# Optimization experiments

Hardware: AMD Instinct MI355X
Metric: run time of the kernel (lower is better)

## Reference

```python
import jax, jax.numpy as jnp
import numpy as np

B, S, HID = 1, 2048, 2048
H = 16
DN, DR, DV = 128, 64, 128          # qk_nope_head_dim, qk_rope_head_dim, v_head_dim
DQ = DN + DR                        # q_head_dim = 192
QLR, KVLR = 1536, 512               # q_lora_rank, kv_lora_rank
MAXP = 32 * 1024
SCALE = DQ ** -0.5
EPS = 1e-6


def rmsnorm(x, w):
    return x * jax.lax.rsqrt(jnp.mean(x * x, axis=-1, keepdims=True) + EPS) * w


def rotate_half(x):
    h = x.shape[-1] // 2
    return jnp.concatenate((-x[..., h:], x[..., :h]), axis=-1)


def interleave_to_half(x):
    # torch: view(b,h,s,d//2,2).transpose(4,3).reshape(b,h,s,d)
    b, h, s, d = x.shape
    return x.reshape(b, h, s, d // 2, 2).transpose(0, 1, 2, 4, 3).reshape(b, h, s, d)


def setup_inputs() -> dict:
    key = jax.random.key(0)
    ks = jax.random.split(key, 8)
    def w(k, shape):
        fan_in = shape[-1]
        return jax.random.normal(k, shape, jnp.float32) * (fan_in ** -0.5)
    inp = {
        "hidden_states": jax.random.normal(ks[0], (B, S, HID), jnp.float32),
        "q_a_w": w(ks[1], (QLR, HID)),
        "q_a_ln": jnp.ones((QLR,), jnp.float32),
        "q_b_w": w(ks[2], (H * DQ, QLR)),
        "kv_a_w": w(ks[3], (KVLR + DR, HID)),
        "kv_a_ln": jnp.ones((KVLR,), jnp.float32),
        "kv_b_w": w(ks[4], (H * (DN + DV), KVLR)),
        "o_w": w(ks[5], (HID, H * DV)),
    }
    # rotary tables, seq_len = 32k
    inv_freq = 1.0 / (10000.0 ** (np.arange(0, DR, 2, dtype=np.float32) / DR))
    t = np.arange(MAXP, dtype=np.float32)
    freqs = np.outer(t, inv_freq)
    emb = np.concatenate((freqs, freqs), axis=-1)
    inp["cos"] = jnp.asarray(np.cos(emb), jnp.float32)
    inp["sin"] = jnp.asarray(np.sin(emb), jnp.float32)
    # bool mask, True = masked (causal)
    inp["attention_mask"] = jnp.triu(jnp.ones((S, S), bool), 1)[None, None]
    inp["position_ids"] = jnp.arange(S, dtype=jnp.int64 if jax.config.jax_enable_x64 else jnp.int32)[None].repeat(B, 0)
    return inp


def reference(hidden_states, q_a_w, q_a_ln, q_b_w, kv_a_w, kv_a_ln, kv_b_w, o_w,
              cos, sin, attention_mask, position_ids):
    b, s, _ = hidden_states.shape
    # low-rank Q: q_b(LN(q_a(x)))
    q = rmsnorm(hidden_states @ q_a_w.T, q_a_ln) @ q_b_w.T         # [b,s,H*DQ]
    q = q.reshape(b, s, H, DQ).transpose(0, 2, 1, 3)               # [b,H,s,DQ]
    q_nope, q_pe = q[..., :DN], q[..., DN:]
    # compressed KV + decoupled rope key
    ckv = hidden_states @ kv_a_w.T                                  # [b,s,KVLR+DR]
    compressed_kv, k_pe = ckv[..., :KVLR], ckv[..., KVLR:]
    k_pe = k_pe.reshape(b, s, 1, DR).transpose(0, 2, 1, 3)          # [b,1,s,DR]
    kv = rmsnorm(compressed_kv, kv_a_ln) @ kv_b_w.T                 # [b,s,H*(DN+DV)]
    kv = kv.reshape(b, s, H, DN + DV).transpose(0, 2, 1, 3)         # [b,H,s,DN+DV]
    k_nope, value_states = kv[..., :DN], kv[..., DN:]
    # rotary with interleaved->half reorder on the rope slice only
    cos_p = cos[position_ids][:, None]                              # [b,1,s,DR]
    sin_p = sin[position_ids][:, None]
    q_pe = interleave_to_half(q_pe)
    k_pe = interleave_to_half(k_pe)
    q_pe = q_pe * cos_p + rotate_half(q_pe) * sin_p
    k_pe = k_pe * cos_p + rotate_half(k_pe) * sin_p
    query_states = jnp.concatenate((q_nope, q_pe), axis=-1)         # [b,H,s,DQ]
    key_states = jnp.concatenate(
        (k_nope, jnp.broadcast_to(k_pe, (b, H, s, DR))), axis=-1)   # [b,H,s,DQ]
    # manual attention
    scores = jnp.einsum("bhqd,bhkd->bhqk", query_states, key_states) * SCALE
    scores = jnp.where(attention_mask, jnp.float32(-10000.0), scores)
    attn = jax.nn.softmax(scores.astype(jnp.float32), axis=-1).astype(query_states.dtype)
    attn_out = jnp.einsum("bhqk,bhkd->bhqd", attn, value_states)    # [b,H,s,DV]
    attn_out = attn_out.transpose(0, 2, 1, 3).reshape(b, s, H * DV)
    return attn_out @ o_w.T                                         # [b,s,HID]
```

## Files before the change

### kernel.cpp

```cpp
#include <hip/hip_runtime.h>
#include <stdint.h>

typedef unsigned short u16;
typedef __attribute__((ext_vector_type(8))) short short8;
typedef __attribute__((ext_vector_type(4))) float f32x4;
typedef __attribute__((ext_vector_type(4))) unsigned short ushort4_t;
typedef __attribute__((ext_vector_type(4))) float float4_t;

#define DEV_INLINE __device__ __forceinline__

DEV_INLINE u16 f2bf(float f) {
    union { float f; unsigned u; } x; x.f = f;
    unsigned u = x.u;
    unsigned r = (u + 0x7FFFu + ((u >> 16) & 1u)) >> 16;
    return (u16)r;
}

DEV_INLINE float bf2f(u16 b) {
    union { unsigned u; float f; } x; x.u = ((unsigned)b) << 16;
    return x.f;
}

DEV_INLINE float fexp2(float x) {
    float r;
    asm("v_exp_f32 %0, %1" : "=v"(r) : "v"(x));
    return r;
}

DEV_INLINE unsigned cvtpk_bf16(float lo, float hi) {
    unsigned r;
    asm("v_cvt_pk_bf16_f32 %0, %1, %2" : "=v"(r) : "v"(lo), "v"(hi));
    return r;
}

template <int CTRL>
DEV_INLINE float dppmaxf(float x) {
    union { float f; int i; } u; u.f = x;
    int y = __builtin_amdgcn_update_dpp(u.i, u.i, CTRL, 0xf, 0xf, true);
    union { int i; float f; } v; v.i = y;
    return fmaxf(x, v.f);
}

DEV_INLINE float dpp_xor1(float x) {
    union { float f; int i; } u; u.f = x;
    int y = __builtin_amdgcn_update_dpp(u.i, u.i, 0xB1, 0xf, 0xf, true);
    union { int i; float f; } v; v.i = y;
    return v.f;
}

DEV_INLINE float rmax16(float x) {
    x = dppmaxf<0xB1>(x);
    x = dppmaxf<0x4E>(x);
    x = dppmaxf<0x141>(x);
    x = dppmaxf<0x140>(x);
    return x;
}

__global__ void conv_all(const float* __restrict__ s0, u16* __restrict__ d0, long e0,
                         const float* __restrict__ s1, u16* __restrict__ d1, long e1,
                         const float* __restrict__ s2, u16* __restrict__ d2, long e2,
                         const float* __restrict__ s3, u16* __restrict__ d3, long e3,
                         const float* __restrict__ s4, u16* __restrict__ d4, long e4,
                         const float* __restrict__ s5, u16* __restrict__ d5, long e5,
                         int rows_valid, int cols4) {
    long i = (long)blockIdx.x * 256 + threadIdx.x;
    if (i >= e5) return;
    if (i >= e4) {
        long j = i - e4;
        long row = j / cols4;
        ushort4_t o; o.x = 0; o.y = 0; o.z = 0; o.w = 0;
        if (row < rows_valid) {
            float4_t v = ((const float4_t*)s5)[j];
            o.x = f2bf(v.x); o.y = f2bf(v.y); o.z = f2bf(v.z); o.w = f2bf(v.w);
        }
        ((ushort4_t*)d5)[j] = o;
        return;
    }
    const float* s; u16* d; long base;
    if      (i < e0) { s = s0; d = d0; base = 0; }
    else if (i < e1) { s = s1; d = d1; base = e0; }
    else if (i < e2) { s = s2; d = d2; base = e1; }
    else if (i < e3) { s = s3; d = d3; base = e2; }
    else             { s = s4; d = d4; base = e3; }
    long j = i - base;
    float4_t v = ((const float4_t*)s)[j];
    ushort4_t o;
    o.x = f2bf(v.x); o.y = f2bf(v.y); o.z = f2bf(v.z); o.w = f2bf(v.w);
    ((ushort4_t*)d)[j] = o;
}

#define BK 32

DEV_INLINE void gload16(const u16* g, u16* l) {
    __builtin_amdgcn_global_load_lds((const __attribute__((address_space(1))) unsigned int*)g,
                                     (__attribute__((address_space(3))) unsigned int*)l,
                                     16, 0, 0);
}

template <typename OT>
__global__ __launch_bounds__(256) void gemm64_db(const u16* __restrict__ A, const u16* __restrict__ B,
                                                 OT* __restrict__ C, int M, int N, int K) {
    __shared__ u16 As[2][64 * BK];
    __shared__ u16 Bs[2][128 * BK];
    const int tid = threadIdx.x;
    const int wid = tid >> 6, lane = tid & 63;
    const int lm = lane & 15, lk = lane >> 4;
    const long bm = (long)blockIdx.y * 64, bn = (long)blockIdx.x * 128;

    f32x4 acc[4][2] = {};

    const int rowS = lane >> 2;
    const int colS = ((lane & 3) ^ ((lane >> 3) & 3)) * 8;
    const int cs = (lm >> 1) & 3;
    const u16* Ag = A + (bm + wid * 16 + rowS) * (long)K + colS;
    const u16* Bg = B + (bn + wid * 32 + rowS) * (long)K + colS;
    const int aoff = wid * 16 * BK;
    const int boff = wid * 32 * BK;

    gload16(Ag, &As[0][aoff]);
    gload16(Bg, &Bs[0][boff]);
    gload16(Bg + 16 * (long)K, &Bs[0][boff + 16 * BK]);
    __syncthreads();

    int cur = 0;
    for (int k0 = 0; k0 < K; k0 += BK) {
        if (k0 + BK < K) {
            gload16(Ag + k0 + BK, &As[cur ^ 1][aoff]);
            gload16(Bg + k0 + BK, &Bs[cur ^ 1][boff]);
            gload16(Bg + 16 * (long)K + k0 + BK, &Bs[cur ^ 1][boff + 16 * BK]);
        }
        short8 af[4], bfr[2];
#pragma unroll
        for (int m = 0; m < 4; ++m)
            af[m] = *(const short8*)&As[cur][(m * 16 + lm) * BK + (lk ^ cs) * 8];
#pragma unroll
        for (int n = 0; n < 2; ++n)
            bfr[n] = *(const short8*)&Bs[cur][(wid * 32 + n * 16 + lm) * BK + (lk ^ cs) * 8];
#pragma unroll
        for (int m = 0; m < 4; ++m)
#pragma unroll
            for (int n = 0; n < 2; ++n)
                acc[m][n] = __builtin_amdgcn_mfma_f32_16x16x32_bf16(af[m], bfr[n], acc[m][n], 0, 0, 0);
        __syncthreads();
        cur ^= 1;
    }

#pragma unroll
    for (int m = 0; m < 4; ++m)
#pragma unroll
        for (int n = 0; n < 2; ++n)
#pragma unroll
            for (int r = 0; r < 4; ++r) {
                long idx = (bm + m * 16 + lk * 4 + r) * (long)N + bn + wid * 32 + n * 16 + lm;
                if constexpr (sizeof(OT) == 4) C[idx] = acc[m][n][r];
                else                           C[idx] = f2bf(acc[m][n][r]);
            }
}

__global__ __launch_bounds__(256) void gemm_qkv(const u16* __restrict__ qnA, const u16* __restrict__ qbB,
                                                const u16* __restrict__ kvnA, const u16* __restrict__ kvbB,
                                                u16* __restrict__ Qb, u16* __restrict__ Kb, u16* __restrict__ Vt,
                                                const int* __restrict__ pos,
                                                const float* __restrict__ cosT, const float* __restrict__ sinT) {
    __shared__ u16 SMEM[12288];
    u16* As = SMEM;
    u16* Bs = SMEM + 4096;
    const int tid = threadIdx.x;
    const int wid = tid >> 6, lane = tid & 63;
    const int lm = lane & 15, lk = lane >> 4;

    const bool isq = blockIdx.x < 768;
    const int gx = isq ? blockIdx.x : blockIdx.x - 768;
    const int nb = isq ? 24 : 32;
    const int K  = isq ? 1536 : 512;
    const u16* A = isq ? qnA : kvnA;
    const u16* B = isq ? qbB : kvbB;
    const long bn = (long)(gx % nb) * 128;
    const long bm = (long)(gx / nb) * 64;

    f32x4 acc[4][2] = {};

    const int rowS = lane >> 2;
    const int colS = ((lane & 3) ^ ((lane >> 3) & 3)) * 8;
    const int cs = (lm >> 1) & 3;
    const u16* Ag = A + (bm + wid * 16 + rowS) * (long)K + colS;
    const u16* Bg = B + (bn + wid * 32 + rowS) * (long)K + colS;
    const int aoff = wid * 16 * BK;
    const int boff = wid * 32 * BK;

    gload16(Ag, &As[aoff]);
    gload16(Bg, &Bs[boff]);
    gload16(Bg + 16 * (long)K, &Bs[boff + 16 * BK]);
    __syncthreads();

    int cur = 0;
    for (int k0 = 0; k0 < K; k0 += BK) {
        if (k0 + BK < K) {
            gload16(Ag + k0 + BK, &As[(cur ^ 1) * 2048 + aoff]);
            gload16(Bg + k0 + BK, &Bs[(cur ^ 1) * 4096 + boff]);
            gload16(Bg + 16 * (long)K + k0 + BK, &Bs[(cur ^ 1) * 4096 + boff + 16 * BK]);
        }
        short8 af[4], bfr[2];
#pragma unroll
        for (int m = 0; m < 4; ++m)
            af[m] = *(const short8*)&As[cur * 2048 + (m * 16 + lm) * BK + (lk ^ cs) * 8];
#pragma unroll
        for (int n = 0; n < 2; ++n)
            bfr[n] = *(const short8*)&Bs[cur * 4096 + (wid * 32 + n * 16 + lm) * BK + (lk ^ cs) * 8];
#pragma unroll
        for (int m = 0; m < 4; ++m)
#pragma unroll
            for (int n = 0; n < 2; ++n)
                acc[m][n] = __builtin_amdgcn_mfma_f32_16x16x32_bf16(af[m], bfr[n], acc[m][n], 0, 0, 0);
        __syncthreads();
        cur ^= 1;
    }

    if (isq) {
#pragma unroll
        for (int n = 0; n < 2; ++n) {
            const int c = (int)bn + wid * 32 + n * 16 + lm;
            const int h = c / 192;
            const int d = c - h * 192;
            const bool pe = (d >= 128);
            const int t = (d - 128) >> 1;
#pragma unroll
            for (int m = 0; m < 4; ++m)
#pragma unroll
                for (int r = 0; r < 4; ++r) {
                    const long row = bm + m * 16 + lk * 4 + r;
                    float own = acc[m][n][r];
                    float par = dpp_xor1(own);
                    float val = own;
                    if (pe) {
                        long p = pos[row];
                        float cc = cosT[p * 64 + t];
                        float ss = sinT[p * 64 + t];
                        val = (d & 1) ? own * cc + par * ss : own * cc - par * ss;
                    }
                    Qb[((long)h * 2048 + row) * 192 + d] = f2bf(val);
                }
        }
    } else {
        const int hh = (gx & 31) >> 1;
        const bool isV = (gx & 1) != 0;
        if (!isV) {
#pragma unroll
            for (int m = 0; m < 4; ++m)
#pragma unroll
                for (int n = 0; n < 2; ++n)
#pragma unroll
                    for (int r = 0; r < 4; ++r)
                        Kb[((long)hh * 2048 + bm + m * 16 + lk * 4 + r) * 192 + wid * 32 + n * 16 + lm]
                            = f2bf(acc[m][n][r]);
        } else {
            __syncthreads();
            u16* Ls = SMEM;
#pragma unroll
            for (int n = 0; n < 2; ++n) {
                int d = wid * 32 + n * 16 + lm;
                int swz = ((d >> 3) & 7) << 3;
#pragma unroll
                for (int m = 0; m < 4; ++m)
#pragma unroll
                    for (int r = 0; r < 4; ++r) {
                        int row = m * 16 + lk * 4 + r;
                        Ls[d * 72 + (row ^ swz)] = f2bf(acc[m][n][r]);
                    }
            }
            __syncthreads();
#pragma unroll
            for (int i = 0; i < 8; ++i) {
                int u = i * 256 + tid;
                int d = u >> 4, s4 = (u & 15) * 4;
                int swz = ((d >> 3) & 7) << 3;
                ushort4_t v;
                v.x = Ls[d * 72 + ((s4 + 0) ^ swz)]; v.y = Ls[d * 72 + ((s4 + 1) ^ swz)];
                v.z = Ls[d * 72 + ((s4 + 2) ^ swz)]; v.w = Ls[d * 72 + ((s4 + 3) ^ swz)];
                *(ushort4_t*)(Vt + ((long)hh * 128 + d) * 2048 + bm + s4) = v;
            }
        }
    }
}

__global__ __launch_bounds__(256) void norm_rope(const float* __restrict__ qkva,
                                                 const float* __restrict__ q_ln,
                                                 const float* __restrict__ kv_ln,
                                                 u16* __restrict__ qn, u16* __restrict__ kvn,
                                                 const int* __restrict__ pos,
                                                 const float* __restrict__ cosT,
                                                 const float* __restrict__ sinT,
                                                 u16* __restrict__ Kb) {
    const int b = blockIdx.x, tid = threadIdx.x;
    if (b < 4096) {
        const bool isq = b < 2048;
        const int row = isq ? b : b - 2048;
        const int ncols = isq ? 1536 : 512;
        const float* x = qkva + (long)row * 2176 + (isq ? 0 : 1536);
        const float* w = isq ? q_ln : kv_ln;
        u16* out = isq ? (qn + (long)row * 1536) : (kvn + (long)row * 512);
        float ss = 0.f;
        for (int c = tid; c < ncols; c += 256) { float v = x[c]; ss = fmaf(v, v, ss); }
#pragma unroll
        for (int off = 32; off > 0; off >>= 1) ss += __shfl_down(ss, off);
        __shared__ float part[4];
        if ((tid & 63) == 0) part[tid >> 6] = ss;
        __syncthreads();
        float tot = part[0] + part[1] + part[2] + part[3];
        float rs = rsqrtf(tot / (float)ncols + 1e-6f);
        for (int c = tid; c < ncols; c += 256) out[c] = f2bf(x[c] * rs * w[c]);
    } else {
        int idx = (b - 4096) * 256 + tid;
        int s = idx >> 5, j = idx & 31;
        long p = pos[s];
        const float* row = qkva + (long)s * 2176 + 2048;
        float x0 = row[2 * j], x1 = row[2 * j + 1];
        float c0 = cosT[p * 64 + j], s0 = sinT[p * 64 + j];
        u16 o0 = f2bf(x0 * c0 - x1 * s0);
        u16 o1 = f2bf(x1 * c0 + x0 * s0);
#pragma unroll
        for (int h = 0; h < 16; ++h) {
            u16* kr = Kb + ((long)h * 2048 + s) * 192 + 128;
            kr[2 * j] = o0; kr[2 * j + 1] = o1;
        }
    }
}

__global__ __launch_bounds__(512) void attn_fwd(const u16* __restrict__ Qb, const u16* __restrict__ Kb,
                                                const u16* __restrict__ Vt, u16* __restrict__ Ao) {
    __shared__ __align__(16) char smem[92672];

    const int b = blockIdx.x;
    const int h = (b & 7) * 2 + ((b >> 3) & 1);
    const int pi = b >> 4;
    const int tid = threadIdx.x;
    const int wid = tid >> 6, lane = tid & 63;
    const int lm = lane & 15, lk = lane >> 4;
    const int s = wid >> 2, wp = wid & 3;
    const int t256 = tid & 255;

    u16* Ks0 = (u16*)smem + s * 12288;
    u16* Vs0 = (u16*)(smem + 49152) + s * 8192;
    u16* PsW = (u16*)(smem + 81920) + wid * 640;
    float* ML = (float*)(smem + 92160);
    float* Ob = (float*)smem;

    const u16* Kh = Kb + (long)h * 2048 * 192;
    const u16* Vh = Vt + (long)h * 128 * 2048;

    short8 bones = {};
    if (lm == 0) {
#pragma unroll
        for (int j = 0; j < 8; ++j) bones[j] = (short)0x3F80;
    }
    const float C2 = 0.104117548f;

    for (int half = 0; half < 2; ++half) {
        const int qi = half ? (31 - pi) : pi;
        const int q0 = qi * 64;
        const int nt = 2 * qi + 2;
        const int niter = qi + 1;

        short8 qf[6];
        const u16* qbase = Qb + ((long)h * 2048 + q0 + wp * 16 + lm) * 192;
#pragma unroll
        for (int kf = 0; kf < 6; ++kf) qf[kf] = *(const short8*)(qbase + kf * 32 + lk * 8);

        f32x4 o[8] = {};
        f32x4 o9 = {};
        float mrow[4] = {-1e30f, -1e30f, -1e30f, -1e30f};

        short8 kreg[3], vreg[2];
        {
            const long k0 = s * 32;
#pragma unroll
            for (int i = 0; i < 3; ++i) {
                int idx = i * 256 + t256; int r = idx / 24, c = (idx % 24) * 8;
                kreg[i] = *(const short8*)(Kh + (k0 + r) * 192 + c);
            }
#pragma unroll
            for (int i = 0; i < 2; ++i) {
                int idx = i * 256 + t256; int dv = idx >> 2, kvb = idx & 3;
                vreg[i] = *(const short8*)(Vh + (long)dv * 2048 + k0 + kvb * 8);
            }
#pragma unroll
            for (int i = 0; i < 3; ++i) {
                int idx = i * 256 + t256; int r = idx / 24, c8 = idx % 24;
                *(short8*)&Ks0[r * 192 + ((c8 ^ (r & 7)) << 3)] = kreg[i];
            }
#pragma unroll
            for (int i = 0; i < 2; ++i) {
                int idx = i * 256 + t256; int dv = idx >> 2, kvb = idx & 3;
                *(short8*)&Vs0[kvb * 1024 + ((dv * 8) ^ (kvb * 16))] = vreg[i];
            }
        }
        __syncthreads();

        int cur = 0;
        for (int it = 0; it < niter; ++it) {
            const int ts = 2 * it + s;
            const int k0 = ts * 32;
            const bool more = (it + 1 < niter);

            if (more) {
                const long k0n = (long)(ts + 2) * 32;
#pragma unroll
                for (int i = 0; i < 3; ++i) {
                    int idx = i * 256 + t256; int r = idx / 24, c = (idx % 24) * 8;
                    kreg[i] = *(const short8*)(Kh + (k0n + r) * 192 + c);
                }
#pragma unroll
                for (int i = 0; i < 2; ++i) {
                    int idx = i * 256 + t256; int dv = idx >> 2, kvb = idx & 3;
                    vreg[i] = *(const short8*)(Vh + (long)dv * 2048 + k0n + kvb * 8);
                }
            }

            const u16* KsC = Ks0 + cur * 6144;
            const u16* VsC = Vs0 + cur * 4096;

            f32x4 sfr[2] = {};
#pragma unroll
            for (int n = 0; n < 2; ++n)
#pragma unroll
                for (int kf = 0; kf < 6; ++kf) {
                    short8 kb = *(const short8*)&KsC[(n * 16 + lm) * 192 + (((kf * 4 + lk) ^ (lm & 7)) << 3)];
                    sfr[n] = __builtin_amdgcn_mfma_f32_16x16x32_bf16(qf[kf], kb, sfr[n], 0, 0, 0);
                }

            float sv[2][4];
            const bool bt = (ts >= nt - 2);
#pragma unroll
            for (int n = 0; n < 2; ++n)
#pragma unroll
                for (int r = 0; r < 4; ++r) {
                    float val = sfr[n][r] * C2;
                    if (bt && (k0 + n * 16 + lm > q0 + wp * 16 + lk * 4 + r)) val = -1e30f;
                    sv[n][r] = val;
                }

            float pmax[4];
#pragma unroll
            for (int r = 0; r < 4; ++r)
                pmax[r] = rmax16(fmaxf(sv[0][r], sv[1][r]));
            bool need = (pmax[0] > mrow[0] + 8.f) || (pmax[1] > mrow[1] + 8.f) ||
                        (pmax[2] > mrow[2] + 8.f) || (pmax[3] > mrow[3] + 8.f);
            if (__any(need)) {
#pragma unroll
                for (int r = 0; r < 4; ++r) {
                    float mnew = fmaxf(mrow[r], pmax[r]);
                    float alpha = fexp2(mrow[r] - mnew);
                    mrow[r] = mnew;
#pragma unroll
                    for (int d = 0; d < 8; ++d) o[d][r] *= alpha;
                    o9[r] *= alpha;
                }
            }
#pragma unroll
            for (int n = 0; n < 2; ++n) {
                float p0 = fexp2(sv[n][0] - mrow[0]);
                float p1 = fexp2(sv[n][1] - mrow[1]);
                float p2 = fexp2(sv[n][2] - mrow[2]);
                float p3 = fexp2(sv[n][3] - mrow[3]);
                unsigned pk01 = cvtpk_bf16(p0, p1);
                unsigned pk23 = cvtpk_bf16(p2, p3);
                int rb = (lk * 4) * 40 + n * 16 + lm;
                PsW[rb]       = (u16)pk01;
                PsW[rb + 40]  = (u16)(pk01 >> 16);
                PsW[rb + 80]  = (u16)pk23;
                PsW[rb + 120] = (u16)(pk23 >> 16);
            }

            short8 pf = *(const short8*)&PsW[lm * 40 + lk * 8];
#pragma unroll
            for (int d = 0; d < 8; ++d) {
                short8 vf = *(const short8*)&VsC[lk * 1024 + (((d * 16 + lm) * 8) ^ (lk * 16))];
                o[d] = __builtin_amdgcn_mfma_f32_16x16x32_bf16(pf, vf, o[d], 0, 0, 0);
            }
            o9 = __builtin_amdgcn_mfma_f32_16x16x32_bf16(pf, bones, o9, 0, 0, 0);

            if (more) {
                u16* KsN = Ks0 + (cur ^ 1) * 6144;
                u16* VsN = Vs0 + (cur ^ 1) * 4096;
#pragma unroll
                for (int i = 0; i < 3; ++i) {
                    int idx = i * 256 + t256; int r = idx / 24, c8 = idx % 24;
                    *(short8*)&KsN[r * 192 + ((c8 ^ (r & 7)) << 3)] = kreg[i];
                }
#pragma unroll
                for (int i = 0; i < 2; ++i) {
                    int idx = i * 256 + t256; int dv = idx >> 2, kvb = idx & 3;
                    *(short8*)&VsN[kvb * 1024 + ((dv * 8) ^ (kvb * 16))] = vreg[i];
                }
            }
            __syncthreads();
            cur ^= 1;
        }

        if (s == 1) {
#pragma unroll
            for (int d = 0; d < 8; ++d)
#pragma unroll
                for (int r = 0; r < 4; ++r)
                    Ob[(wp * 16 + lk * 4 + r) * 128 + d * 16 + lm] = o[d][r];
            if (lm == 0) {
#pragma unroll
                for (int r = 0; r < 4; ++r) {
                    int row = wp * 16 + lk * 4 + r;
                    ML[row * 2 + 0] = mrow[r];
                    ML[row * 2 + 1] = o9[r];
                }
            }
        }
        __syncthreads();
        if (s == 0) {
            float e0[4], e1[4], invl[4];
#pragma unroll
            for (int r = 0; r < 4; ++r) {
                int row = wp * 16 + lk * 4 + r;
                float m1 = ML[row * 2 + 0];
                float l1 = ML[row * 2 + 1];
                float l0 = __shfl(o9[r], lane & 48);
                float M = fmaxf(mrow[r], m1);
                e0[r] = fexp2(mrow[r] - M);
                e1[r] = fexp2(m1 - M);
                invl[r] = 1.f / (l0 * e0[r] + l1 * e1[r]);
            }
#pragma unroll
            for (int d = 0; d < 8; ++d)
#pragma unroll
                for (int r = 0; r < 4; ++r) {
                    int row = wp * 16 + lk * 4 + r;
                    float val = (o[d][r] * e0[r] +
                                 Ob[row * 128 + d * 16 + lm] * e1[r]) * invl[r];
                    Ao[((long)q0 + row) * 2048 + h * 128 + d * 16 + lm] = f2bf(val);
                }
        }
        __syncthreads();
    }
}

extern "C" void kernel_launch(void* const* d_in, const int* in_sizes, int n_in,
                              void* d_out, int out_size, void* d_ws, size_t ws_size,
                              hipStream_t stream) {
    (void)in_sizes; (void)n_in; (void)out_size; (void)ws_size;
    const float* hidden  = (const float*)d_in[0];
    const float* q_a_w   = (const float*)d_in[1];
    const float* q_a_ln  = (const float*)d_in[2];
    const float* q_b_w   = (const float*)d_in[3];
    const float* kv_a_w  = (const float*)d_in[4];
    const float* kv_a_ln = (const float*)d_in[5];
    const float* kv_b_w  = (const float*)d_in[6];
    const float* o_w     = (const float*)d_in[7];
    const float* cosT    = (const float*)d_in[8];
    const float* sinT    = (const float*)d_in[9];
    const int*   pos     = (const int*)d_in[11];

    char* ws = (char*)d_ws;
    u16* o_w_bf   = (u16*)(ws + 0);
    u16* qb_w_bf  = (u16*)(ws + 8388608);
    u16* kvb_w_bf = (u16*)(ws + 17825792);
    u16* qn_bf    = (u16*)(ws + 22020096);
    u16* kvn_bf   = (u16*)(ws + 28311552);
    u16* Qb       = (u16*)(ws + 30408704);
    u16* Kb       = (u16*)(ws + 42991616);
    u16* Vt       = (u16*)(ws + 55574528);
    u16* aout_bf  = (u16*)(ws + 63963136);
    u16*   hid_bf    = (u16*)(ws + 72351744);
    u16*   qkva_w_bf = (u16*)(ws + 80740352);
    float* qkva_f    = (float*)(ws + 89653248);

    conv_all<<<19200, 256, 0, stream>>>(
        hidden, hid_bf,                 1048576L,
        q_a_w,  qkva_w_bf,              1835008L,
        q_b_w,  qb_w_bf,                3014656L,
        kv_b_w, kvb_w_bf,               3538944L,
        o_w,    o_w_bf,                 4587520L,
        kv_a_w, qkva_w_bf + 1536L*2048, 4915200L,
        576, 512);

    gemm64_db<float><<<dim3(17, 32), 256, 0, stream>>>(hid_bf, qkva_w_bf, qkva_f, 2048, 2176, 2048);

    norm_rope<<<4352, 256, 0, stream>>>(qkva_f, q_a_ln, kv_a_ln, qn_bf, kvn_bf, pos, cosT, sinT, Kb);

    gemm_qkv<<<1792, 256, 0, stream>>>(qn_bf, qb_w_bf, kvn_bf, kvb_w_bf, Qb, Kb, Vt, pos, cosT, sinT);

    attn_fwd<<<256, 512, 0, stream>>>(Qb, Kb, Vt, aout_bf);

    gemm64_db<float><<<dim3(16, 32), 256, 0, stream>>>(aout_bf, o_w_bf, (float*)d_out, 2048, 2048, 2048);
}
```

Before: 223.2 us.

## Fuse fp32-to-bf16 conversion into GEMM tile loads, drop standalone convert kernel

Removes the separate conversion kernel that turned the inputs and all weights into bf16 copies. Each GEMM now loads fp32 operands straight from global memory into registers, converts them with packed bf16 instructions, and writes them to LDS after the MFMA step, keeping the double-buffer overlap. This saves one launch and a full extra read/write pass over roughly 20M elements. In exchange, each GEMM tile reads twice the bytes per operand and weight tiles are reloaded and reconverted by every block row, and the async global-to-LDS loads become register-staged loads.

```diff
diff --git a/kernel.cpp b/kernel.cpp
--- a/kernel.cpp
+++ b/kernel.cpp
@@ -6,6 +6,7 @@
 typedef __attribute__((ext_vector_type(4))) float f32x4;
 typedef __attribute__((ext_vector_type(4))) unsigned short ushort4_t;
 typedef __attribute__((ext_vector_type(4))) float float4_t;
+typedef __attribute__((ext_vector_type(4))) unsigned uint4_t;
 
 #define DEV_INLINE __device__ __forceinline__
 
@@ -16,11 +17,6 @@
     return (u16)r;
 }
 
-DEV_INLINE float bf2f(u16 b) {
-    union { unsigned u; float f; } x; x.u = ((unsigned)b) << 16;
-    return x.f;
-}
-
 DEV_INLINE float fexp2(float x) {
     float r;
     asm("v_exp_f32 %0, %1" : "=v"(r) : "v"(x));
@@ -31,6 +27,15 @@
     unsigned r;
     asm("v_cvt_pk_bf16_f32 %0, %1, %2" : "=v"(r) : "v"(lo), "v"(hi));
     return r;
+}
+
+DEV_INLINE void cvt_store8(u16* dst, float4_t lo, float4_t hi) {
+    uint4_t w;
+    w.x = cvtpk_bf16(lo.x, lo.y);
+    w.y = cvtpk_bf16(lo.z, lo.w);
+    w.z = cvtpk_bf16(hi.x, hi.y);
+    w.w = cvtpk_bf16(hi.z, hi.w);
+    *(uint4_t*)dst = w;
 }
 
 template <int CTRL>
@@ -56,39 +61,6 @@
     return x;
 }
 
-__global__ void conv_all(const float* __restrict__ s0, u16* __restrict__ d0, long e0,
-                         const float* __restrict__ s1, u16* __restrict__ d1, long e1,
-                         const float* __restrict__ s2, u16* __restrict__ d2, long e2,
-                         const float* __restrict__ s3, u16* __restrict__ d3, long e3,
-                         const float* __restrict__ s4, u16* __restrict__ d4, long e4,
-                         const float* __restrict__ s5, u16* __restrict__ d5, long e5,
-                         int rows_valid, int cols4) {
-    long i = (long)blockIdx.x * 256 + threadIdx.x;
-    if (i >= e5) return;
-    if (i >= e4) {
-        long j = i - e4;
-        long row = j / cols4;
-        ushort4_t o; o.x = 0; o.y = 0; o.z = 0; o.w = 0;
-        if (row < rows_valid) {
-            float4_t v = ((const float4_t*)s5)[j];
-            o.x = f2bf(v.x); o.y = f2bf(v.y); o.z = f2bf(v.z); o.w = f2bf(v.w);
-        }
-        ((ushort4_t*)d5)[j] = o;
-        return;
-    }
-    const float* s; u16* d; long base;
-    if      (i < e0) { s = s0; d = d0; base = 0; }
-    else if (i < e1) { s = s1; d = d1; base = e0; }
-    else if (i < e2) { s = s2; d = d2; base = e1; }
-    else if (i < e3) { s = s3; d = d3; base = e2; }
-    else             { s = s4; d = d4; base = e3; }
-    long j = i - base;
-    float4_t v = ((const float4_t*)s)[j];
-    ushort4_t o;
-    o.x = f2bf(v.x); o.y = f2bf(v.y); o.z = f2bf(v.z); o.w = f2bf(v.w);
-    ((ushort4_t*)d)[j] = o;
-}
-
 #define BK 32
 
 DEV_INLINE void gload16(const u16* g, u16* l) {
@@ -97,37 +69,125 @@
                                      16, 0, 0);
 }
 
-template <typename OT>
-__global__ __launch_bounds__(256) void gemm64_db(const u16* __restrict__ A, const u16* __restrict__ B,
-                                                 OT* __restrict__ C, int M, int N, int K) {
+__global__ __launch_bounds__(256) void gemm_down(const float* __restrict__ hid,
+                                                 const float* __restrict__ qaw,
+                                                 const float* __restrict__ kvaw,
+                                                 float* __restrict__ C) {
     __shared__ u16 As[2][64 * BK];
     __shared__ u16 Bs[2][128 * BK];
     const int tid = threadIdx.x;
     const int wid = tid >> 6, lane = tid & 63;
     const int lm = lane & 15, lk = lane >> 4;
     const long bm = (long)blockIdx.y * 64, bn = (long)blockIdx.x * 128;
+    const int K = 2048;
 
     f32x4 acc[4][2] = {};
-
+    const int rowS = lane >> 2;
+    const int colS = ((lane & 3) ^ ((lane >> 3) & 3)) * 8;
+    const int cs = (lm >> 1) & 3;
+
+    const float* Ag = hid + (bm + wid * 16 + rowS) * (long)K + colS;
+    const long r0 = bn + wid * 32 + rowS;
+    const long r1 = r0 + 16;
+    const float* Bg0 = (r0 < 1536) ? qaw + r0 * 2048 + colS
+                      : ((r0 - 1536) < 576 ? kvaw + (r0 - 1536) * 2048 + colS : nullptr);
+    const float* Bg1 = (r1 < 1536) ? qaw + r1 * 2048 + colS
+                      : ((r1 - 1536) < 576 ? kvaw + (r1 - 1536) * 2048 + colS : nullptr);
+    const int aoff = wid * 16 * BK + lane * 8;
+    const int boff0 = wid * 32 * BK + lane * 8;
+    const int boff1 = boff0 + 16 * BK;
+
+    const float4_t zf = {0.f, 0.f, 0.f, 0.f};
+    float4_t a0, a1, b00, b01, b10, b11;
+
+#define LOADT(k0)                                                                                  \
+    a0 = *(const float4_t*)(Ag + (k0));                                                            \
+    a1 = *(const float4_t*)(Ag + (k0) + 4);                                                        \
+    if (Bg0) { b00 = *(const float4_t*)(Bg0 + (k0)); b01 = *(const float4_t*)(Bg0 + (k0) + 4); }   \
+    else     { b00 = zf; b01 = zf; }                                                               \
+    if (Bg1) { b10 = *(const float4_t*)(Bg1 + (k0)); b11 = *(const float4_t*)(Bg1 + (k0) + 4); }   \
+    else     { b10 = zf; b11 = zf; }
+
+    LOADT(0);
+    cvt_store8(&As[0][aoff], a0, a1);
+    cvt_store8(&Bs[0][boff0], b00, b01);
+    cvt_store8(&Bs[0][boff1], b10, b11);
+    __syncthreads();
+
+    int cur = 0;
+    for (int k0 = 0; k0 < K; k0 += BK) {
+        const bool more = (k0 + BK < K);
+        if (more) { LOADT(k0 + BK); }
+        short8 af[4], bfr[2];
+#pragma unroll
+        for (int m = 0; m < 4; ++m)
+            af[m] = *(const short8*)&As[cur][(m * 16 + lm) * BK + (lk ^ cs) * 8];
+#pragma unroll
+        for (int n = 0; n < 2; ++n)
+            bfr[n] = *(const short8*)&Bs[cur][(wid * 32 + n * 16 + lm) * BK + (lk ^ cs) * 8];
+#pragma unroll
+        for (int m = 0; m < 4; ++m)
+#pragma unroll
+            for (int n = 0; n < 2; ++n)
+                acc[m][n] = __builtin_amdgcn_mfma_f32_16x16x32_bf16(af[m], bfr[n], acc[m][n], 0, 0, 0);
+        if (more) {
+            cvt_store8(&As[cur ^ 1][aoff], a0, a1);
+            cvt_store8(&Bs[cur ^ 1][boff0], b00, b01);
+            cvt_store8(&Bs[cur ^ 1][boff1], b10, b11);
+        }
+        __syncthreads();
+        cur ^= 1;
+    }
+#undef LOADT
+
+#pragma unroll
+    for (int m = 0; m < 4; ++m)
+#pragma unroll
+        for (int n = 0; n < 2; ++n)
+#pragma unroll
+            for (int r = 0; r < 4; ++r)
+                C[(bm + m * 16 + lk * 4 + r) * 2176L + bn + wid * 32 + n * 16 + lm] = acc[m][n][r];
+}
+
+__global__ __launch_bounds__(256) void gemm_o(const u16* __restrict__ A, const float* __restrict__ B,
+                                              float* __restrict__ C, int M, int N, int K) {
+    __shared__ u16 As[2][64 * BK];
+    __shared__ u16 Bs[2][128 * BK];
+    const int tid = threadIdx.x;
+    const int wid = tid >> 6, lane = tid & 63;
+    const int lm = lane & 15, lk = lane >> 4;
+    const long bm = (long)blockIdx.y * 64, bn = (long)blockIdx.x * 128;
+
+    f32x4 acc[4][2] = {};
     const int rowS = lane >> 2;
     const int colS = ((lane & 3) ^ ((lane >> 3) & 3)) * 8;
     const int cs = (lm >> 1) & 3;
     const u16* Ag = A + (bm + wid * 16 + rowS) * (long)K + colS;
-    const u16* Bg = B + (bn + wid * 32 + rowS) * (long)K + colS;
+    const float* Bg0 = B + (bn + wid * 32 + rowS) * (long)K + colS;
+    const float* Bg1 = Bg0 + 16 * (long)K;
     const int aoff = wid * 16 * BK;
-    const int boff = wid * 32 * BK;
+    const int boff0 = wid * 32 * BK + lane * 8;
+    const int boff1 = boff0 + 16 * BK;
+
+    float4_t b00, b01, b10, b11;
+#define LOADB(k0)                                        \
+    b00 = *(const float4_t*)(Bg0 + (k0));                \
+    b01 = *(const float4_t*)(Bg0 + (k0) + 4);            \
+    b10 = *(const float4_t*)(Bg1 + (k0));                \
+    b11 = *(const float4_t*)(Bg1 + (k0) + 4);
 
     gload16(Ag, &As[0][aoff]);
-    gload16(Bg, &Bs[0][boff]);
-    gload16(Bg + 16 * (long)K, &Bs[0][boff + 16 * BK]);
+    LOADB(0);
+    cvt_store8(&Bs[0][boff0], b00, b01);
+    cvt_store8(&Bs[0][boff1], b10, b11);
     __syncthreads();
 
     int cur = 0;
     for (int k0 = 0; k0 < K; k0 += BK) {
-        if (k0 + BK < K) {
+        const bool more = (k0 + BK < K);
+        if (more) {
             gload16(Ag + k0 + BK, &As[cur ^ 1][aoff]);
-            gload16(Bg + k0 + BK, &Bs[cur ^ 1][boff]);
-            gload16(Bg + 16 * (long)K + k0 + BK, &Bs[cur ^ 1][boff + 16 * BK]);
+            LOADB(k0 + BK);
         }
         short8 af[4], bfr[2];
 #pragma unroll
@@ -141,24 +201,26 @@
 #pragma unroll
             for (int n = 0; n < 2; ++n)
                 acc[m][n] = __builtin_amdgcn_mfma_f32_16x16x32_bf16(af[m], bfr[n], acc[m][n], 0, 0, 0);
+        if (more) {
+            cvt_store8(&Bs[cur ^ 1][boff0], b00, b01);
+            cvt_store8(&Bs[cur ^ 1][boff1], b10, b11);
+        }
         __syncthreads();
         cur ^= 1;
     }
+#undef LOADB
 
 #pragma unroll
     for (int m = 0; m < 4; ++m)
 #pragma unroll
         for (int n = 0; n < 2; ++n)
 #pragma unroll
-            for (int r = 0; r < 4; ++r) {
-                long idx = (bm + m * 16 + lk * 4 + r) * (long)N + bn + wid * 32 + n * 16 + lm;
-                if constexpr (sizeof(OT) == 4) C[idx] = acc[m][n][r];
-                else                           C[idx] = f2bf(acc[m][n][r]);
-            }
-}
-
-__global__ __launch_bounds__(256) void gemm_qkv(const u16* __restrict__ qnA, const u16* __restrict__ qbB,
-                                                const u16* __restrict__ kvnA, const u16* __restrict__ kvbB,
+            for (int r = 0; r < 4; ++r)
+                C[(bm + m * 16 + lk * 4 + r) * (long)N + bn + wid * 32 + n * 16 + lm] = acc[m][n][r];
+}
+
+__global__ __launch_bounds__(256) void gemm_qkv(const u16* __restrict__ qnA, const float* __restrict__ qbw,
+                                                const u16* __restrict__ kvnA, const float* __restrict__ kvbw,
                                                 u16* __restrict__ Qb, u16* __restrict__ Kb, u16* __restrict__ Vt,
                                                 const int* __restrict__ pos,
                                                 const float* __restrict__ cosT, const float* __restrict__ sinT) {
@@ -174,7 +236,7 @@
     const int nb = isq ? 24 : 32;
     const int K  = isq ? 1536 : 512;
     const u16* A = isq ? qnA : kvnA;
-    const u16* B = isq ? qbB : kvbB;
+    const float* Bf = isq ? qbw : kvbw;
     const long bn = (long)(gx % nb) * 128;
     const long bm = (long)(gx / nb) * 64;
 
@@ -184,21 +246,31 @@
     const int colS = ((lane & 3) ^ ((lane >> 3) & 3)) * 8;
     const int cs = (lm >> 1) & 3;
     const u16* Ag = A + (bm + wid * 16 + rowS) * (long)K + colS;
-    const u16* Bg = B + (bn + wid * 32 + rowS) * (long)K + colS;
+    const float* Bg0 = Bf + (bn + wid * 32 + rowS) * (long)K + colS;
+    const float* Bg1 = Bg0 + 16 * (long)K;
     const int aoff = wid * 16 * BK;
-    const int boff = wid * 32 * BK;
+    const int boff0 = wid * 32 * BK + lane * 8;
+    const int boff1 = boff0 + 16 * BK;
+
+    float4_t b00, b01, b10, b11;
+#define LOADB(k0)                                        \
+    b00 = *(const float4_t*)(Bg0 + (k0));                \
+    b01 = *(const float4_t*)(Bg0 + (k0) + 4);            \
+    b10 = *(const float4_t*)(Bg1 + (k0));                \
+    b11 = *(const float4_t*)(Bg1 + (k0) + 4);
 
     gload16(Ag, &As[aoff]);
-    gload16(Bg, &Bs[boff]);
-    gload16(Bg + 16 * (long)K, &Bs[boff + 16 * BK]);
+    LOADB(0);
+    cvt_store8(&Bs[boff0], b00, b01);
+    cvt_store8(&Bs[boff1], b10, b11);
     __syncthreads();
 
     int cur = 0;
     for (int k0 = 0; k0 < K; k0 += BK) {
-        if (k0 + BK < K) {
+        const bool more = (k0 + BK < K);
+        if (more) {
             gload16(Ag + k0 + BK, &As[(cur ^ 1) * 2048 + aoff]);
-            gload16(Bg + k0 + BK, &Bs[(cur ^ 1) * 4096 + boff]);
-            gload16(Bg + 16 * (long)K + k0 + BK, &Bs[(cur ^ 1) * 4096 + boff + 16 * BK]);
+            LOADB(k0 + BK);
         }
         short8 af[4], bfr[2];
 #pragma unroll
@@ -212,9 +284,14 @@
 #pragma unroll
             for (int n = 0; n < 2; ++n)
                 acc[m][n] = __builtin_amdgcn_mfma_f32_16x16x32_bf16(af[m], bfr[n], acc[m][n], 0, 0, 0);
+        if (more) {
+            cvt_store8(&Bs[(cur ^ 1) * 4096 + boff0], b00, b01);
+            cvt_store8(&Bs[(cur ^ 1) * 4096 + boff1], b10, b11);
+        }
         __syncthreads();
         cur ^= 1;
     }
+#undef LOADB
 
     if (isq) {
 #pragma unroll
@@ -557,35 +634,21 @@
     const int*   pos     = (const int*)d_in[11];
 
     char* ws = (char*)d_ws;
-    u16* o_w_bf   = (u16*)(ws + 0);
-    u16* qb_w_bf  = (u16*)(ws + 8388608);
-    u16* kvb_w_bf = (u16*)(ws + 17825792);
-    u16* qn_bf    = (u16*)(ws + 22020096);
-    u16* kvn_bf   = (u16*)(ws + 28311552);
-    u16* Qb       = (u16*)(ws + 30408704);
-    u16* Kb       = (u16*)(ws + 42991616);
-    u16* Vt       = (u16*)(ws + 55574528);
-    u16* aout_bf  = (u16*)(ws + 63963136);
-    u16*   hid_bf    = (u16*)(ws + 72351744);
-    u16*   qkva_w_bf = (u16*)(ws + 80740352);
-    float* qkva_f    = (float*)(ws + 89653248);
-
-    conv_all<<<19200, 256, 0, stream>>>(
-        hidden, hid_bf,                 1048576L,
-        q_a_w,  qkva_w_bf,              1835008L,
-        q_b_w,  qb_w_bf,                3014656L,
-        kv_b_w, kvb_w_bf,               3538944L,
-        o_w,    o_w_bf,                 4587520L,
-        kv_a_w, qkva_w_bf + 1536L*2048, 4915200L,
-        576, 512);
-
-    gemm64_db<float><<<dim3(17, 32), 256, 0, stream>>>(hid_bf, qkva_w_bf, qkva_f, 2048, 2176, 2048);
+    u16*   qn_bf  = (u16*)(ws + 0);
+    u16*   kvn_bf = (u16*)(ws + 6291456);
+    u16*   Qb     = (u16*)(ws + 8388608);
+    u16*   Kb     = (u16*)(ws + 20971520);
+    u16*   Vt     = (u16*)(ws + 33554432);
+    u16*   aout_bf= (u16*)(ws + 41943040);
+    float* qkva_f = (float*)(ws + 50331648);
+
+    gemm_down<<<dim3(17, 32), 256, 0, stream>>>(hidden, q_a_w, kv_a_w, qkva_f);
 
     norm_rope<<<4352, 256, 0, stream>>>(qkva_f, q_a_ln, kv_a_ln, qn_bf, kvn_bf, pos, cosT, sinT, Kb);
 
-    gemm_qkv<<<1792, 256, 0, stream>>>(qn_bf, qb_w_bf, kvn_bf, kvb_w_bf, Qb, Kb, Vt, pos, cosT, sinT);
+    gemm_qkv<<<1792, 256, 0, stream>>>(qn_bf, q_b_w, kvn_bf, kv_b_w, Qb, Kb, Vt, pos, cosT, sinT);
 
     attn_fwd<<<256, 512, 0, stream>>>(Qb, Kb, Vt, aout_bf);
 
-    gemm64_db<float><<<dim3(16, 32), 256, 0, stream>>>(aout_bf, o_w_bf, (float*)d_out, 2048, 2048, 2048);
-}
+    gemm_o<<<dim3(16, 32), 256, 0, stream>>>(aout_bf, o_w, (float*)d_out, 2048, 2048, 2048);
+}
```

Measured after the change: 237.5 us. 1.06x slower.

## Split attention q-tile pairs into separate blocks and single-buffer K/V LDS

Applied to the files above, without the earlier changes.

Each attention block previously processed a causally balanced pair of 64-row query tiles in sequence. Now each block handles one tile, and the grid doubles to 512 blocks, with the first 256 taking the short tiles and the rest the long ones. LDS double buffering is replaced by a single buffer behind an extra barrier, cutting shared memory from about 92KB to 51KB so two 512-thread blocks can be resident per CU. The trade is the loss of overlap between LDS stores and compute, an extra sync per iteration, and less even per-block work.

```diff
diff --git a/kernel.cpp b/kernel.cpp
--- a/kernel.cpp
+++ b/kernel.cpp
@@ -14,11 +14,6 @@
     unsigned u = x.u;
     unsigned r = (u + 0x7FFFu + ((u >> 16) & 1u)) >> 16;
     return (u16)r;
-}
-
-DEV_INLINE float bf2f(u16 b) {
-    union { unsigned u; float f; } x; x.u = ((unsigned)b) << 16;
-    return x.f;
 }
 
 DEV_INLINE float fexp2(float x) {
@@ -328,21 +323,23 @@
 
 __global__ __launch_bounds__(512) void attn_fwd(const u16* __restrict__ Qb, const u16* __restrict__ Kb,
                                                 const u16* __restrict__ Vt, u16* __restrict__ Ao) {
-    __shared__ __align__(16) char smem[92672];
+    __shared__ __align__(16) char smem[51712];
 
     const int b = blockIdx.x;
-    const int h = (b & 7) * 2 + ((b >> 3) & 1);
-    const int pi = b >> 4;
+    const int u = b & 255;
+    const int h = (u & 7) * 2 + ((u >> 3) & 1);
+    const int bq = u >> 4;
+    const int qi = (b < 256) ? bq : 31 - bq;
     const int tid = threadIdx.x;
     const int wid = tid >> 6, lane = tid & 63;
     const int lm = lane & 15, lk = lane >> 4;
     const int s = wid >> 2, wp = wid & 3;
     const int t256 = tid & 255;
 
-    u16* Ks0 = (u16*)smem + s * 12288;
-    u16* Vs0 = (u16*)(smem + 49152) + s * 8192;
-    u16* PsW = (u16*)(smem + 81920) + wid * 640;
-    float* ML = (float*)(smem + 92160);
+    u16* KsS = (u16*)smem + s * 6144;
+    u16* VsS = (u16*)(smem + 24576) + s * 4096;
+    u16* PsW = (u16*)(smem + 40960) + wid * 640;
+    float* ML = (float*)(smem + 51200);
     float* Ob = (float*)smem;
 
     const u16* Kh = Kb + (long)h * 2048 * 192;
@@ -355,188 +352,178 @@
     }
     const float C2 = 0.104117548f;
 
-    for (int half = 0; half < 2; ++half) {
-        const int qi = half ? (31 - pi) : pi;
-        const int q0 = qi * 64;
-        const int nt = 2 * qi + 2;
-        const int niter = qi + 1;
-
-        short8 qf[6];
-        const u16* qbase = Qb + ((long)h * 2048 + q0 + wp * 16 + lm) * 192;
-#pragma unroll
-        for (int kf = 0; kf < 6; ++kf) qf[kf] = *(const short8*)(qbase + kf * 32 + lk * 8);
-
-        f32x4 o[8] = {};
-        f32x4 o9 = {};
-        float mrow[4] = {-1e30f, -1e30f, -1e30f, -1e30f};
-
-        short8 kreg[3], vreg[2];
-        {
-            const long k0 = s * 32;
+    const int q0 = qi * 64;
+    const int nt = 2 * qi + 2;
+    const int niter = qi + 1;
+
+    short8 qf[6];
+    const u16* qbase = Qb + ((long)h * 2048 + q0 + wp * 16 + lm) * 192;
+#pragma unroll
+    for (int kf = 0; kf < 6; ++kf) qf[kf] = *(const short8*)(qbase + kf * 32 + lk * 8);
+
+    f32x4 o[8] = {};
+    f32x4 o9 = {};
+    float mrow[4] = {-1e30f, -1e30f, -1e30f, -1e30f};
+
+    short8 kreg[3], vreg[2];
+    {
+        const long k0 = s * 32;
+#pragma unroll
+        for (int i = 0; i < 3; ++i) {
+            int idx = i * 256 + t256; int r = idx / 24, c = (idx % 24) * 8;
+            kreg[i] = *(const short8*)(Kh + (k0 + r) * 192 + c);
+        }
+#pragma unroll
+        for (int i = 0; i < 2; ++i) {
+            int idx = i * 256 + t256; int dv = idx >> 2, kvb = idx & 3;
+            vreg[i] = *(const short8*)(Vh + (long)dv * 2048 + k0 + kvb * 8);
+        }
+#pragma unroll
+        for (int i = 0; i < 3; ++i) {
+            int idx = i * 256 + t256; int r = idx / 24, c8 = idx % 24;
+            *(short8*)&KsS[r * 192 + ((c8 ^ (r & 7)) << 3)] = kreg[i];
+        }
+#pragma unroll
+        for (int i = 0; i < 2; ++i) {
+            int idx = i * 256 + t256; int dv = idx >> 2, kvb = idx & 3;
+            *(short8*)&VsS[kvb * 1024 + ((dv * 8) ^ (kvb * 16))] = vreg[i];
+        }
+    }
+    __syncthreads();
+
+    for (int it = 0; it < niter; ++it) {
+        const int ts = 2 * it + s;
+        const int k0 = ts * 32;
+        const bool more = (it + 1 < niter);
+
+        if (more) {
+            const long k0n = (long)(ts + 2) * 32;
 #pragma unroll
             for (int i = 0; i < 3; ++i) {
                 int idx = i * 256 + t256; int r = idx / 24, c = (idx % 24) * 8;
-                kreg[i] = *(const short8*)(Kh + (k0 + r) * 192 + c);
+                kreg[i] = *(const short8*)(Kh + (k0n + r) * 192 + c);
             }
 #pragma unroll
             for (int i = 0; i < 2; ++i) {
                 int idx = i * 256 + t256; int dv = idx >> 2, kvb = idx & 3;
-                vreg[i] = *(const short8*)(Vh + (long)dv * 2048 + k0 + kvb * 8);
-            }
+                vreg[i] = *(const short8*)(Vh + (long)dv * 2048 + k0n + kvb * 8);
+            }
+        }
+
+        f32x4 sfr[2] = {};
+#pragma unroll
+        for (int n = 0; n < 2; ++n)
+#pragma unroll
+            for (int kf = 0; kf < 6; ++kf) {
+                short8 kb = *(const short8*)&KsS[(n * 16 + lm) * 192 + (((kf * 4 + lk) ^ (lm & 7)) << 3)];
+                sfr[n] = __builtin_amdgcn_mfma_f32_16x16x32_bf16(qf[kf], kb, sfr[n], 0, 0, 0);
+            }
+
+        float sv[2][4];
+        const bool bt = (ts >= nt - 2);
+#pragma unroll
+        for (int n = 0; n < 2; ++n)
+#pragma unroll
+            for (int r = 0; r < 4; ++r) {
+                float val = sfr[n][r] * C2;
+                if (bt && (k0 + n * 16 + lm > q0 + wp * 16 + lk * 4 + r)) val = -1e30f;
+                sv[n][r] = val;
+            }
+
+        float pmax[4];
+#pragma unroll
+        for (int r = 0; r < 4; ++r)
+            pmax[r] = rmax16(fmaxf(sv[0][r], sv[1][r]));
+        bool need = (pmax[0] > mrow[0] + 8.f) || (pmax[1] > mrow[1] + 8.f) ||
+                    (pmax[2] > mrow[2] + 8.f) || (pmax[3] > mrow[3] + 8.f);
+        if (__any(need)) {
+#pragma unroll
+            for (int r = 0; r < 4; ++r) {
+                float mnew = fmaxf(mrow[r], pmax[r]);
+                float alpha = fexp2(mrow[r] - mnew);
+                mrow[r] = mnew;
+#pragma unroll
+                for (int d = 0; d < 8; ++d) o[d][r] *= alpha;
+                o9[r] *= alpha;
+            }
+        }
+#pragma unroll
+        for (int n = 0; n < 2; ++n) {
+            float p0 = fexp2(sv[n][0] - mrow[0]);
+            float p1 = fexp2(sv[n][1] - mrow[1]);
+            float p2 = fexp2(sv[n][2] - mrow[2]);
+            float p3 = fexp2(sv[n][3] - mrow[3]);
+            unsigned pk01 = cvtpk_bf16(p0, p1);
+            unsigned pk23 = cvtpk_bf16(p2, p3);
+            int rb = (lk * 4) * 40 + n * 16 + lm;
+            PsW[rb]       = (u16)pk01;
+            PsW[rb + 40]  = (u16)(pk01 >> 16);
+            PsW[rb + 80]  = (u16)pk23;
+            PsW[rb + 120] = (u16)(pk23 >> 16);
+        }
+
+        short8 pf = *(const short8*)&PsW[lm * 40 + lk * 8];
+#pragma unroll
+        for (int d = 0; d < 8; ++d) {
+            short8 vf = *(const short8*)&VsS[lk * 1024 + (((d * 16 + lm) * 8) ^ (lk * 16))];
+            o[d] = __builtin_amdgcn_mfma_f32_16x16x32_bf16(pf, vf, o[d], 0, 0, 0);
+        }
+        o9 = __builtin_amdgcn_mfma_f32_16x16x32_bf16(pf, bones, o9, 0, 0, 0);
+
+        __syncthreads();
+        if (more) {
 #pragma unroll
             for (int i = 0; i < 3; ++i) {
                 int idx = i * 256 + t256; int r = idx / 24, c8 = idx % 24;
-                *(short8*)&Ks0[r * 192 + ((c8 ^ (r & 7)) << 3)] = kreg[i];
+                *(short8*)&KsS[r * 192 + ((c8 ^ (r & 7)) << 3)] = kreg[i];
             }
 #pragma unroll
             for (int i = 0; i < 2; ++i) {
                 int idx = i * 256 + t256; int dv = idx >> 2, kvb = idx & 3;
-                *(short8*)&Vs0[kvb * 1024 + ((dv * 8) ^ (kvb * 16))] = vreg[i];
+                *(short8*)&VsS[kvb * 1024 + ((dv * 8) ^ (kvb * 16))] = vreg[i];
             }
         }
         __syncthreads();
-
-        int cur = 0;
-        for (int it = 0; it < niter; ++it) {
-            const int ts = 2 * it + s;
-            const int k0 = ts * 32;
-            const bool more = (it + 1 < niter);
-
-            if (more) {
-                const long k0n = (long)(ts + 2) * 32;
-#pragma unroll
-                for (int i = 0; i < 3; ++i) {
-                    int idx = i * 256 + t256; int r = idx / 24, c = (idx % 24) * 8;
-                    kreg[i] = *(const short8*)(Kh + (k0n + r) * 192 + c);
-                }
-#pragma unroll
-                for (int i = 0; i < 2; ++i) {
-                    int idx = i * 256 + t256; int dv = idx >> 2, kvb = idx & 3;
-                    vreg[i] = *(const short8*)(Vh + (long)dv * 2048 + k0n + kvb * 8);
-                }
-            }
-
-            const u16* KsC = Ks0 + cur * 6144;
-            const u16* VsC = Vs0 + cur * 4096;
-
-            f32x4 sfr[2] = {};
-#pragma unroll
-            for (int n = 0; n < 2; ++n)
-#pragma unroll
-                for (int kf = 0; kf < 6; ++kf) {
-                    short8 kb = *(const short8*)&KsC[(n * 16 + lm) * 192 + (((kf * 4 + lk) ^ (lm & 7)) << 3)];
-                    sfr[n] = __builtin_amdgcn_mfma_f32_16x16x32_bf16(qf[kf], kb, sfr[n], 0, 0, 0);
-                }
-
-            float sv[2][4];
-            const bool bt = (ts >= nt - 2);
-#pragma unroll
-            for (int n = 0; n < 2; ++n)
-#pragma unroll
-                for (int r = 0; r < 4; ++r) {
-                    float val = sfr[n][r] * C2;
-                    if (bt && (k0 + n * 16 + lm > q0 + wp * 16 + lk * 4 + r)) val = -1e30f;
-                    sv[n][r] = val;
-                }
-
-            float pmax[4];
+    }
+
+    if (s == 1) {
+#pragma unroll
+        for (int d = 0; d < 8; ++d)
 #pragma unroll
             for (int r = 0; r < 4; ++r)
-                pmax[r] = rmax16(fmaxf(sv[0][r], sv[1][r]));
-            bool need = (pmax[0] > mrow[0] + 8.f) || (pmax[1] > mrow[1] + 8.f) ||
-                        (pmax[2] > mrow[2] + 8.f) || (pmax[3] > mrow[3] + 8.f);
-            if (__any(need)) {
-#pragma unroll
-                for (int r = 0; r < 4; ++r) {
-                    float mnew = fmaxf(mrow[r], pmax[r]);
-                    float alpha = fexp2(mrow[r] - mnew);
-                    mrow[r] = mnew;
-#pragma unroll
-                    for (int d = 0; d < 8; ++d) o[d][r] *= alpha;
-                    o9[r] *= alpha;
-                }
-            }
-#pragma unroll
-            for (int n = 0; n < 2; ++n) {
-                float p0 = fexp2(sv[n][0] - mrow[0]);
-                float p1 = fexp2(sv[n][1] - mrow[1]);
-                float p2 = fexp2(sv[n][2] - mrow[2]);
-                float p3 = fexp2(sv[n][3] - mrow[3]);
-                unsigned pk01 = cvtpk_bf16(p0, p1);
-                unsigned pk23 = cvtpk_bf16(p2, p3);
-                int rb = (lk * 4) * 40 + n * 16 + lm;
-                PsW[rb]       = (u16)pk01;
-                PsW[rb + 40]  = (u16)(pk01 >> 16);
-                PsW[rb + 80]  = (u16)pk23;
-                PsW[rb + 120] = (u16)(pk23 >> 16);
-            }
-
-            short8 pf = *(const short8*)&PsW[lm * 40 + lk * 8];
-#pragma unroll
-            for (int d = 0; d < 8; ++d) {
-                short8 vf = *(const short8*)&VsC[lk * 1024 + (((d * 16 + lm) * 8) ^ (lk * 16))];
-                o[d] = __builtin_amdgcn_mfma_f32_16x16x32_bf16(pf, vf, o[d], 0, 0, 0);
-            }
-            o9 = __builtin_amdgcn_mfma_f32_16x16x32_bf16(pf, bones, o9, 0, 0, 0);
-
-            if (more) {
-                u16* KsN = Ks0 + (cur ^ 1) * 6144;
-                u16* VsN = Vs0 + (cur ^ 1) * 4096;
-#pragma unroll
-                for (int i = 0; i < 3; ++i) {
-                    int idx = i * 256 + t256; int r = idx / 24, c8 = idx % 24;
-                    *(short8*)&KsN[r * 192 + ((c8 ^ (r & 7)) << 3)] = kreg[i];
-                }
-#pragma unroll
-                for (int i = 0; i < 2; ++i) {
-                    int idx = i * 256 + t256; int dv = idx >> 2, kvb = idx & 3;
-                    *(short8*)&VsN[kvb * 1024 + ((dv * 8) ^ (kvb * 16))] = vreg[i];
-                }
-            }
-            __syncthreads();
-            cur ^= 1;
-        }
-
-        if (s == 1) {
-#pragma unroll
-            for (int d = 0; d < 8; ++d)
-#pragma unroll
-                for (int r = 0; r < 4; ++r)
-                    Ob[(wp * 16 + lk * 4 + r) * 128 + d * 16 + lm] = o[d][r];
-            if (lm == 0) {
-#pragma unroll
-                for (int r = 0; r < 4; ++r) {
-                    int row = wp * 16 + lk * 4 + r;
-                    ML[row * 2 + 0] = mrow[r];
-                    ML[row * 2 + 1] = o9[r];
-                }
-            }
-        }
-        __syncthreads();
-        if (s == 0) {
-            float e0[4], e1[4], invl[4];
+                Ob[(wp * 16 + lk * 4 + r) * 128 + d * 16 + lm] = o[d][r];
+        if (lm == 0) {
 #pragma unroll
             for (int r = 0; r < 4; ++r) {
                 int row = wp * 16 + lk * 4 + r;
-                float m1 = ML[row * 2 + 0];
-                float l1 = ML[row * 2 + 1];
-                float l0 = __shfl(o9[r], lane & 48);
-                float M = fmaxf(mrow[r], m1);
-                e0[r] = fexp2(mrow[r] - M);
-                e1[r] = fexp2(m1 - M);
-                invl[r] = 1.f / (l0 * e0[r] + l1 * e1[r]);
-            }
-#pragma unroll
-            for (int d = 0; d < 8; ++d)
-#pragma unroll
-                for (int r = 0; r < 4; ++r) {
-                    int row = wp * 16 + lk * 4 + r;
-                    float val = (o[d][r] * e0[r] +
-                                 Ob[row * 128 + d * 16 + lm] * e1[r]) * invl[r];
-                    Ao[((long)q0 + row) * 2048 + h * 128 + d * 16 + lm] = f2bf(val);
-                }
-        }
-        __syncthreads();
+                ML[row * 2 + 0] = mrow[r];
+                ML[row * 2 + 1] = o9[r];
+            }
+        }
+    }
+    __syncthreads();
+    if (s == 0) {
+        float e0[4], e1[4], invl[4];
+#pragma unroll
+        for (int r = 0; r < 4; ++r) {
+            int row = wp * 16 + lk * 4 + r;
+            float m1 = ML[row * 2 + 0];
+            float l1 = ML[row * 2 + 1];
+            float l0 = __shfl(o9[r], lane & 48);
+            float M = fmaxf(mrow[r], m1);
+            e0[r] = fexp2(mrow[r] - M);
+            e1[r] = fexp2(m1 - M);
+            invl[r] = 1.f / (l0 * e0[r] + l1 * e1[r]);
+        }
+#pragma unroll
+        for (int d = 0; d < 8; ++d)
+#pragma unroll
+            for (int r = 0; r < 4; ++r) {
+                int row = wp * 16 + lk * 4 + r;
+                float val = (o[d][r] * e0[r] +
+                             Ob[row * 128 + d * 16 + lm] * e1[r]) * invl[r];
+                Ao[((long)q0 + row) * 2048 + h * 128 + d * 16 + lm] = f2bf(val);
+            }
     }
 }
 
@@ -585,7 +572,7 @@
 
     gemm_qkv<<<1792, 256, 0, stream>>>(qn_bf, qb_w_bf, kvn_bf, kvb_w_bf, Qb, Kb, Vt, pos, cosT, sinT);
 
-    attn_fwd<<<256, 512, 0, stream>>>(Qb, Kb, Vt, aout_bf);
+    attn_fwd<<<512, 512, 0, stream>>>(Qb, Kb, Vt, aout_bf);
 
     gemm64_db<float><<<dim3(16, 32), 256, 0, stream>>>(aout_bf, o_w_bf, (float*)d_out, 2048, 2048, 2048);
 }
```

Result: no change. 224.2 us (+0.4%).
